# Kernel tuning notes

Hardware: AMD Instinct MI355X
Metric: run time of the kernel (lower is better)

The kernel has to match this reference:

```python
import jax, jax.numpy as jnp
import numpy as np

N_BATCH = 2; N_RAYS = 4096; S_COARSE = 32; S_FINE = 32
FEATURE_DIM = 32; BOX_WARP = 6.0; EPS = 1e-5

_PLANE_AXES = np.array([[[1, 0, 0], [0, 1, 0], [0, 0, 1]],
                        [[1, 0, 0], [0, 0, 1], [0, 1, 0]],
                        [[0, 0, 1], [0, 1, 0], [1, 0, 0]]], dtype=np.float32)
_INV_PLANES = np.linalg.inv(_PLANE_AXES)  # [3,3,3]


def _grid_sample(feat, coords):
    # feat [B,C,H,W], coords [B,M,2] in [-1,1] (x->W, y->H); bilinear, align_corners=False, zero padding
    B, C, H, W = feat.shape
    x = (coords[..., 0] + 1.0) * (W * 0.5) - 0.5
    y = (coords[..., 1] + 1.0) * (H * 0.5) - 0.5
    x0 = jnp.floor(x); y0 = jnp.floor(y)
    wx = x - x0; wy = y - y0
    x0i = x0.astype(jnp.int32); y0i = y0.astype(jnp.int32)

    def corner(fb, yi, xi):
        valid = ((xi >= 0) & (xi < W) & (yi >= 0) & (yi < H)).astype(fb.dtype)
        v = fb[:, jnp.clip(yi, 0, H - 1), jnp.clip(xi, 0, W - 1)]  # [C,M]
        return v * valid[None, :]

    def one(fb, x0b, y0b, wxb, wyb):
        x1b = x0b + 1; y1b = y0b + 1
        return (corner(fb, y0b, x0b) * (1 - wxb) * (1 - wyb)
                + corner(fb, y0b, x1b) * wxb * (1 - wyb)
                + corner(fb, y1b, x0b) * (1 - wxb) * wyb
                + corner(fb, y1b, x1b) * wxb * wyb)  # [C,M]

    return jax.vmap(one)(feat, x0i, y0i, wx, wy)  # [B,C,M]


def _sample_from_planes(planes, coords):
    # planes [N,3,C,H,W], coords [N,M,3] -> [N,3,M,C]
    N, n_planes, C, H, W = planes.shape
    M = coords.shape[1]
    c = coords * (2.0 / BOX_WARP)
    proj = jnp.einsum('nmc,pcd->npmd', c, jnp.asarray(_INV_PLANES))[..., :2]  # [N,3,M,2]
    out = _grid_sample(planes.reshape(N * n_planes, C, H, W), proj.reshape(N * n_planes, M, 2))
    return out.reshape(N, n_planes, C, M).transpose(0, 1, 3, 2)


def _decoder(feat, W1, b1, W2, b2):
    # OSGDecoder: Linear -> softplus -> Linear; rgb sigmoid-squashed, sigma raw
    h = jax.nn.softplus(feat @ W1 + b1)
    o = h @ W2 + b2
    rgb = jax.nn.sigmoid(o[..., 1:]) * (1 + 2 * 0.001) - 0.001
    sigma = o[..., 0:1]
    return rgb, sigma


def _run_model(planes, coords, W1, b1, W2, b2, beta):
    sf = _sample_from_planes(planes, coords).mean(axis=1)  # [N,M,C]
    rgb, raw_sigma = _decoder(sf, W1, b1, W2, b2)
    pred_sdf = raw_sigma
    # template SDF stand-in (external FLAME tex_feature net): sphere SDF
    tsdf = jnp.linalg.norm(coords, axis=-1, keepdims=True) - 0.5
    sigma = raw_sigma + tsdf
    density = jax.nn.sigmoid(-sigma / beta) / beta  # sdf_activation(-sigma)
    return rgb, density, pred_sdf


def _ray_march(colors, densities, depths):
    deltas = depths[:, :, 1:] - depths[:, :, :-1]
    c_mid = 0.5 * (colors[:, :, :-1] + colors[:, :, 1:])
    d_mid = 0.5 * (densities[:, :, :-1] + densities[:, :, 1:])
    z_mid = 0.5 * (depths[:, :, :-1] + depths[:, :, 1:])
    alpha = 1.0 - jnp.exp(-d_mid * deltas)
    shifted = jnp.concatenate([jnp.ones_like(alpha[:, :, :1]), 1.0 - alpha + 1e-10], axis=2)
    weights = alpha * jnp.cumprod(shifted, axis=2)[:, :, :-1]
    comp_rgb = jnp.sum(weights * c_mid, axis=2) * 2.0 - 1.0
    w_tot = jnp.sum(weights, axis=2)
    comp_depth = jnp.sum(weights * z_mid, axis=2) / w_tot
    comp_depth = jnp.nan_to_num(comp_depth, nan=jnp.inf)
    comp_depth = jnp.clip(comp_depth, depths.min(), depths.max())
    return comp_rgb, comp_depth, weights


def _sample_pdf(bins, weights, u):
    n_w = weights.shape[-1]
    w = weights + EPS
    pdf = w / jnp.sum(w, axis=-1, keepdims=True)
    cdf = jnp.cumsum(pdf, axis=-1)
    cdf = jnp.concatenate([jnp.zeros_like(cdf[:, :1]), cdf], axis=-1)
    inds = jax.vmap(lambda c, uu: jnp.searchsorted(c, uu, side='right'))(cdf, u)
    below = jnp.maximum(inds - 1, 0)
    above = jnp.minimum(inds, n_w)
    cdf0 = jnp.take_along_axis(cdf, below, axis=-1)
    cdf1 = jnp.take_along_axis(cdf, above, axis=-1)
    b0 = jnp.take_along_axis(bins, below, axis=-1)
    b1v = jnp.take_along_axis(bins, above, axis=-1)
    denom = cdf1 - cdf0
    denom = jnp.where(denom < EPS, 1.0, denom)
    return b0 + (u - cdf0) / denom * (b1v - b0)


def _sample_importance(z_vals, weights, u):
    B, R, S, _ = z_vals.shape
    z = z_vals.reshape(B * R, S)
    w = weights.reshape(B * R, -1)  # S-1
    # torch max_pool1d(k=2,s=1,pad=1) then avg_pool1d(k=2,s=1)
    neg = jnp.full_like(w[:, :1], -1e10)
    wp = jnp.concatenate([neg, w, neg], axis=-1)
    m = jnp.maximum(wp[:, :-1], wp[:, 1:])  # len S
    w_sm = 0.5 * (m[:, :-1] + m[:, 1:]) + 0.01  # len S-1
    z_mid = 0.5 * (z[:, :-1] + z[:, 1:])  # len S-1
    s = _sample_pdf(z_mid, w_sm[:, 1:-1], u)
    return jax.lax.stop_gradient(s.reshape(B, R, -1, 1))


def reference(planes, ray_origins, ray_directions, hit_min_depth, hit_max_depth, jitter, u_importance, W1, b1, W2, b2, sigmoid_beta, hit_mask):
    N, M, _ = ray_origins.shape
    beta = jnp.maximum(sigmoid_beta, 0.002)
    mask = hit_mask.astype(planes.dtype)[:, :, None, None]  # [N,M,1,1]
    hmin = jnp.where(mask == 0, hit_min_depth.min(), hit_min_depth)
    hmax = jnp.where(mask == 0, hit_max_depth.max(), hit_max_depth)
    base = jnp.linspace(0.0, 1.0, S_COARSE, dtype=planes.dtype).reshape(1, 1, S_COARSE, 1)
    span = hmax - hmin
    d_coarse = (base + jitter * span / S_COARSE) * span + hmin  # [N,M,S,1]

    def eval_points(depths):
        coords = ray_origins[:, :, None, :] + depths * ray_directions[:, :, None, :]
        S = depths.shape[2]
        rgb, dens, psdf = _run_model(planes, coords.reshape(N, M * S, 3), W1, b1, W2, b2, beta)
        # masked scatter-back into dense buffers == multiply by hit mask
        rgb = rgb.reshape(N, M, S, FEATURE_DIM) * mask
        dens = dens.reshape(N, M, S, 1) * mask
        return rgb, dens, psdf

    rgb_c, dens_c, psdf_c = eval_points(d_coarse)
    _, _, w_c = _ray_march(rgb_c, dens_c, d_coarse)
    d_fine = _sample_importance(d_coarse, w_c, u_importance)
    rgb_f, dens_f, psdf_f = eval_points(d_fine)

    all_d = jnp.concatenate([d_coarse, d_fine], axis=2)
    all_c = jnp.concatenate([rgb_c, rgb_f], axis=2)
    all_s = jnp.concatenate([dens_c, dens_f], axis=2)
    idx = jnp.argsort(all_d, axis=2)
    all_d = jnp.take_along_axis(all_d, idx, axis=2)
    all_c = jnp.take_along_axis(all_c, jnp.broadcast_to(idx, all_c.shape), axis=2)
    all_s = jnp.take_along_axis(all_s, jnp.broadcast_to(idx, all_s.shape), axis=2)

    rgb_final, depth_final, weights = _ray_march(all_c, all_s, all_d)
    all_pred_sdf = jnp.concatenate([psdf_c, psdf_f], axis=1)
    return rgb_final, depth_final, weights, all_pred_sdf


def setup_inputs():
    key = jax.random.key(0)
    ks = jax.random.split(key, 12)
    planes = jax.random.normal(ks[0], (N_BATCH, 3, 32, 256, 256), jnp.float32)
    ray_origins = 0.1 * jax.random.normal(ks[1], (N_BATCH, N_RAYS, 3), jnp.float32)
    rd = jax.random.normal(ks[2], (N_BATCH, N_RAYS, 3), jnp.float32)
    ray_directions = rd / jnp.linalg.norm(rd, axis=-1, keepdims=True)
    hit_min_depth = 0.8 + 0.4 * jax.random.uniform(ks[3], (N_BATCH, N_RAYS, 1, 1), jnp.float32)
    hit_max_depth = hit_min_depth + 0.5 + jax.random.uniform(ks[4], (N_BATCH, N_RAYS, 1, 1), jnp.float32)
    jitter = jax.random.uniform(ks[5], (N_BATCH, N_RAYS, S_COARSE, 1), jnp.float32)
    u_importance = jax.random.uniform(ks[6], (N_BATCH * N_RAYS, S_FINE), jnp.float32)
    W1 = 0.05 * jax.random.normal(ks[7], (32, 64), jnp.float32)
    b1 = jnp.zeros((64,), jnp.float32)
    W2 = 0.05 * jax.random.normal(ks[8], (64, 1 + FEATURE_DIM), jnp.float32)
    b2 = jnp.zeros((1 + FEATURE_DIM,), jnp.float32)
    sigmoid_beta = 0.1 * jnp.ones((1,), jnp.float32)
    hit_mask = jax.random.randint(ks[9], (N_BATCH, N_RAYS), 0, 2, jnp.int32)
    return {'planes': planes, 'ray_origins': ray_origins, 'ray_directions': ray_directions,
            'hit_min_depth': hit_min_depth, 'hit_max_depth': hit_max_depth, 'jitter': jitter,
            'u_importance': u_importance, 'W1': W1, 'b1': b1, 'W2': W2, 'b2': b2,
            'sigmoid_beta': sigmoid_beta, 'hit_mask': hit_mask}
```

## Files before the change

kernel.cpp:

```cpp
#include <hip/hip_runtime.h>
#include <hip/hip_bf16.h>
#include <math.h>
#include <stddef.h>

typedef unsigned int u32;
typedef unsigned short u16;
typedef unsigned long long u64;

#define NRAYS 8192
#define NSAMP 262144

__device__ __forceinline__ float fa(float a,float b){ return __fadd_rn(a,b); }
__device__ __forceinline__ float fs(float a,float b){ return __fsub_rn(a,b); }
__device__ __forceinline__ float fm(float a,float b){ return __fmul_rn(a,b); }
__device__ __forceinline__ float fdv(float a,float b){ return __fdiv_rn(a,b); }

__device__ __forceinline__ double exp_d(double x){
  const double LOG2E  = 1.4426950408889634074;
  const double LN2_HI = 6.93147180369123816490e-01;
  const double LN2_LO = 1.90821492927058770002e-10;
  double kd = rint(x * LOG2E);
  if (kd >  200.0) return INFINITY;
  if (kd < -200.0) return 0.0;
  int k = (int)kd;
  double r = fma(-kd, LN2_HI, x);
  r = fma(-kd, LN2_LO, r);
  double p = 1.0/39916800.0;
  p = fma(p, r, 1.0/3628800.0);
  p = fma(p, r, 1.0/362880.0);
  p = fma(p, r, 1.0/40320.0);
  p = fma(p, r, 1.0/5040.0);
  p = fma(p, r, 1.0/720.0);
  p = fma(p, r, 1.0/120.0);
  p = fma(p, r, 1.0/24.0);
  p = fma(p, r, 1.0/6.0);
  p = fma(p, r, 0.5);
  p = fma(p, r, 1.0);
  p = fma(p, r, 1.0);
  u64 sb = ((u64)(k + 1023)) << 52;
  return p * __longlong_as_double((long long)sb);
}
__device__ __forceinline__ float exf(float x){ return (float)exp_d((double)x); }
__device__ __forceinline__ float sigm(float x){
  if (x >= 0.f){ float e = exf(-x); return fdv(1.f, fa(1.f, e)); }
  float e = exf(x); return fdv(e, fa(1.f, e));
}
__device__ __forceinline__ float sigm_fast(float x){
  return 1.f/(1.f + __expf(-x));
}
__device__ __forceinline__ u16 f2b(float f){
  u32 x = __float_as_uint(f);
  return (u16)((x + 0x7fffu + ((x>>16)&1u)) >> 16);
}
__device__ __forceinline__ u32 fenc(float f){ u32 b=__float_as_uint(f); return (b&0x80000000u)? ~b : (b|0x80000000u); }
__device__ __forceinline__ float fdec(u32 k){ u32 b=(k&0x80000000u)? (k^0x80000000u) : ~k; return __uint_as_float(b); }

__global__ void k_init(const float* __restrict__ hmin, const float* __restrict__ hmax,
                       const float* __restrict__ W1, float* __restrict__ scal,
                       float* __restrict__ W1t){
  __shared__ float smn[256], smx[256];
  int t = threadIdx.x;
  float mn = 1e30f, mx = -1e30f;
  for (int i=t;i<NRAYS;i+=256){ mn=fminf(mn,hmin[i]); mx=fmaxf(mx,hmax[i]); }
  smn[t]=mn; smx[t]=mx; __syncthreads();
  for(int s=128;s>0;s>>=1){
    if(t<s){ smn[t]=fminf(smn[t],smn[t+s]); smx[t]=fmaxf(smx[t],smx[t+s]); }
    __syncthreads();
  }
  if(t==0){
    scal[0]=smn[0]; scal[1]=smx[0];
    ((u32*)scal)[2]=0xFFFFFFFFu;
    ((u32*)scal)[3]=0u;
  }
  for(int i=t;i<2048;i+=256){ int j=i>>5, c=i&31; W1t[i]=W1[c*64+j]; }
}

__global__ void __launch_bounds__(256) k_tr(const float* __restrict__ pl, float* __restrict__ pt){
  int t = blockIdx.x*256 + threadIdx.x;
  int x  = t & 255;
  int c4 = ((t>>8)&7)<<2;
  int y  = (t>>11)&255;
  int np = t>>19;
  const float* ip = pl + (((size_t)(np*32+c4))<<16) + (y<<8) + x;
  float4 o;
  o.x = ip[0];
  o.y = ip[65536];
  o.z = ip[131072];
  o.w = ip[196608];
  *reinterpret_cast<float4*>(pt + ((((size_t)(np<<8|y))<<8|x)<<5) + c4) = o;
}

template<int PHASE>
__global__ void __launch_bounds__(256) k_eval(
  const float* __restrict__ pt, const float* __restrict__ ro, const float* __restrict__ rd,
  const float* __restrict__ hmin, const float* __restrict__ hmax,
  const float* __restrict__ jitter, const int* __restrict__ hitmask,
  const float* __restrict__ W1t, const float* __restrict__ b1,
  const float* __restrict__ W2, const float* __restrict__ b2,
  const float* __restrict__ sb, float* __restrict__ scal,
  float* __restrict__ dep, float* __restrict__ dens_out, u16* __restrict__ rgb_out,
  float* __restrict__ out_psdf)
{
  int idx = blockIdx.x*256 + threadIdx.x;
  int ray = idx >> 5;
  int s   = idx & 31;
  int n   = ray >> 12;
  int msk = hitmask[ray];

  float d;
  if (PHASE==0){
    float hmn = msk ? hmin[ray] : scal[0];
    float hmx = msk ? hmax[ray] : scal[1];
    float span = fs(hmx, hmn);
    float jit  = jitter[idx];
    float base = (float)((double)s * (1.0/31.0));
    if (s==31) base = 1.0f;
    float t1 = fdv(fm(jit, span), 32.0f);
    d = fa(fm(fa(base, t1), span), hmn);
    dep[idx] = d;
    float dm=d, dM=d;
#pragma unroll
    for (int m=1;m<64;m<<=1){ dm=fminf(dm,__shfl_xor(dm,m)); dM=fmaxf(dM,__shfl_xor(dM,m)); }
    if ((threadIdx.x & 63)==0){
      atomicMin(((u32*)scal)+2, fenc(dm));
      atomicMax(((u32*)scal)+3, fenc(dM));
    }
  } else {
    d = dep[idx];
  }

  float ox=ro[ray*3+0], oy=ro[ray*3+1], oz=ro[ray*3+2];
  float dx=rd[ray*3+0], dy=rd[ray*3+1], dz=rd[ray*3+2];
  float px = fa(ox, fm(d,dx)), py = fa(oy, fm(d,dy)), pz = fa(oz, fm(d,dz));
  float nrm = __fsqrt_rn(fa(fa(fm(px,px),fm(py,py)),fm(pz,pz)));
  float tsdf = fs(nrm, 0.5f);
  const float sc2 = (float)(2.0/6.0);
  float cx=fm(px,sc2), cy=fm(py,sc2), cz=fm(pz,sc2);

  float feat[32];
#pragma unroll
  for(int c=0;c<32;c++) feat[c]=0.f;

#pragma unroll
  for (int p=0;p<3;p++){
    float u = (p==2)?cz:cx;
    float v = (p==1)?cz:cy;
    float fx = fs(fm(fa(u,1.f),128.f),0.5f);
    float fy = fs(fm(fa(v,1.f),128.f),0.5f);
    float x0f = floorf(fx), y0f = floorf(fy);
    float wx = fs(fx,x0f), wy = fs(fy,y0f);
    float ax0 = fs(1.f,wx), ax1 = wx, ay0 = fs(1.f,wy), ay1 = wy;
    int x0, y0;
    {
      x0 = (x0f >= 2.1e9f) ? 2147483647 : ((x0f <= -2.1e9f) ? (-2147483647-1) : (int)x0f);
      y0 = (y0f >= 2.1e9f) ? 2147483647 : ((y0f <= -2.1e9f) ? (-2147483647-1) : (int)y0f);
    }
    int x1=x0+1, y1=y0+1;
    bool vx0 = (x0>=0 && x0<256), vx1 = (x1>=0 && x1<256);
    bool vy0 = (y0>=0 && y0<256), vy1 = (y1>=0 && y1<256);
    bool ok00 = vx0&&vy0, ok01 = vx1&&vy0, ok10 = vx0&&vy1, ok11 = vx1&&vy1;
    int cx0=min(max(x0,0),255), cx1=min(max(x1,0),255);
    int cy0=min(max(y0,0),255), cy1=min(max(y1,0),255);
    int npl = n*3+p;
    size_t pb = ((size_t)npl)<<16;
    const float4* t00 = (const float4*)(pt + ((pb + (cy0<<8) + cx0)<<5));
    const float4* t01 = (const float4*)(pt + ((pb + (cy0<<8) + cx1)<<5));
    const float4* t10 = (const float4*)(pt + ((pb + (cy1<<8) + cx0)<<5));
    const float4* t11 = (const float4*)(pt + ((pb + (cy1<<8) + cx1)<<5));
#pragma unroll
    for(int q=0;q<8;q++){
      float4 v00 = t00[q], v01 = t01[q], v10 = t10[q], v11 = t11[q];
      float e0,e1,e2,e3, t_;
#define CORNER_SUM(FLD, OUTI) \
      e0 = ok00 ? v00.FLD : 0.f; e1 = ok01 ? v01.FLD : 0.f; \
      e2 = ok10 ? v10.FLD : 0.f; e3 = ok11 ? v11.FLD : 0.f; \
      t_ = fa(fa(fa(fm(fm(e0,ax0),ay0), fm(fm(e1,ax1),ay0)), fm(fm(e2,ax0),ay1)), fm(fm(e3,ax1),ay1)); \
      feat[q*4+OUTI] = fa(feat[q*4+OUTI], t_);
      CORNER_SUM(x,0) CORNER_SUM(y,1) CORNER_SUM(z,2) CORNER_SUM(w,3)
#undef CORNER_SUM
    }
  }
#pragma unroll
  for(int c=0;c<32;c++) feat[c] = fdv(feat[c], 3.0f);

  float o[33];
#pragma unroll
  for(int k=0;k<33;k++) o[k]=0.f;
#pragma unroll 2
  for(int j=0;j<64;j++){
    float a = 0.f;
#pragma unroll
    for(int c=0;c<32;c++) a = fmaf(feat[c], W1t[j*32+c], a);
    a = fa(a, b1[j]);
    float h = fa(fmaxf(a,0.f), __logf(fa(1.f, __expf(-fabsf(a)))));
#pragma unroll
    for(int k=0;k<33;k++) o[k] = fmaf(h, W2[j*33+k], o[k]);
  }
#pragma unroll
  for(int k=0;k<33;k++) o[k] = fa(o[k], b2[k]);

  float beta = fmaxf(sb[0], 0.002f);
  float raw = o[0];
  out_psdf[((size_t)n<<18) + ((size_t)PHASE<<17) + (size_t)(ray&4095)*32 + s] = raw;
  float sg = fa(raw, tsdf);
  float dens = msk ? fdv(sigm(fdv(-sg, beta)), beta) : 0.f;
  dens_out[idx]=dens;

  u16 rv[32];
#pragma unroll
  for(int c=0;c<32;c++){
    float r = msk ? fs(fm(sigm_fast(o[c+1]), 1.002f), 0.001f) : 0.f;
    rv[c]=f2b(r);
  }
  uint4* op = (uint4*)(rgb_out + (size_t)idx*32);
#pragma unroll
  for(int q=0;q<4;q++){
    uint4 w;
    w.x = (u32)rv[q*8+0] | ((u32)rv[q*8+1]<<16);
    w.y = (u32)rv[q*8+2] | ((u32)rv[q*8+3]<<16);
    w.z = (u32)rv[q*8+4] | ((u32)rv[q*8+5]<<16);
    w.w = (u32)rv[q*8+6] | ((u32)rv[q*8+7]<<16);
    op[q]=w;
  }
}

__global__ void __launch_bounds__(64) k_imp(
  const float* __restrict__ dc, const float* __restrict__ dens,
  const float* __restrict__ u_imp, float* __restrict__ df, float* __restrict__ scal)
{
  __shared__ float scdf[64][30];
  __shared__ float szm [64][30];
  int tid = threadIdx.x;
  int ray = blockIdx.x*64 + tid;
  float w[31];
  float dprev = dc[ray*32+0];
  float sprev = dens[ray*32+0];
  float T = 1.f;
#pragma unroll
  for(int i=0;i<31;i++){
    float dn = dc[ray*32+i+1];
    float sn = dens[ray*32+i+1];
    if (i<30) szm[tid][i] = fm(0.5f, fa(dprev,dn));
    float delta = fs(dn,dprev);
    float dm = fm(0.5f, fa(sprev,sn));
    float al = fs(1.f, exf(-fm(dm,delta)));
    w[i] = fm(al,T);
    T = fm(T, fa(fs(1.f,al), 1e-10f));
    dprev=dn; sprev=sn;
  }
  float pdfw[29];
#pragma unroll
  for(int i=0;i<29;i++){
    float m1 = fmaxf(w[i],w[i+1]), m2 = fmaxf(w[i+1],w[i+2]);
    pdfw[i] = fa(fa(fm(0.5f, fa(m1,m2)), 0.01f), 1e-5f);
  }
  float sum;
  {
    float r[8];
#pragma unroll
    for(int j=0;j<8;j++) r[j]=pdfw[j];
#pragma unroll
    for(int j=0;j<8;j++) r[j]=fa(r[j],pdfw[8+j]);
#pragma unroll
    for(int j=0;j<8;j++) r[j]=fa(r[j],pdfw[16+j]);
    sum = fa(fa(fa(r[0],r[1]),fa(r[2],r[3])), fa(fa(r[4],r[5]),fa(r[6],r[7])));
#pragma unroll
    for(int i=24;i<29;i++) sum = fa(sum, pdfw[i]);
  }
  {
    float cacc = 0.f;
    scdf[tid][0] = 0.f;
#pragma unroll
    for(int i=1;i<30;i++){
      cacc = fa(cacc, fdv(pdfw[i-1], sum));
      scdf[tid][i] = cacc;
    }
  }

  float fmn=1e30f, fmx=-1e30f;
  for(int k=0;k<32;k++){
    float u = u_imp[ray*32+k];
    int lo=0, hi=30;
    while(lo<hi){
      int mid=(lo+hi)>>1;
      if (scdf[tid][mid] <= u) lo = mid+1; else hi = mid;
    }
    int ind = lo;
    int below = ind-1;
    int above = (ind>29)?29:ind;
    float cdf0 = scdf[tid][below];
    float cdf1 = scdf[tid][above];
    float b0   = szm [tid][below];
    float b1v  = szm [tid][above];
    float den = fs(cdf1,cdf0);
    if((double)den < 1e-5) den = 1.f;
    float sres = fa(b0, fm(fdv(fs(u,cdf0),den), fs(b1v,b0)));
    df[ray*32+k]=sres;
    fmn=fminf(fmn,sres); fmx=fmaxf(fmx,sres);
  }
#pragma unroll
  for(int m=1;m<64;m<<=1){ fmn=fminf(fmn,__shfl_xor(fmn,m)); fmx=fmaxf(fmx,__shfl_xor(fmx,m)); }
  if(tid==0){
    atomicMin(((u32*)scal)+2, fenc(fmn));
    atomicMax(((u32*)scal)+3, fenc(fmx));
  }
}

__global__ void __launch_bounds__(256) k_final(
  const float* __restrict__ dc, const float* __restrict__ df,
  const float* __restrict__ densc, const float* __restrict__ densf,
  const u16* __restrict__ rgbc, const u16* __restrict__ rgbf,
  const float* __restrict__ scal,
  float* __restrict__ out_rgb, float* __restrict__ out_depth, float* __restrict__ out_w)
{
  __shared__ float ssd[4][64];
  __shared__ float ssn[4][64];
  __shared__ int   sp [4][64];
  __shared__ float swv[4][64];
  __shared__ float swz[4][64];
  int wid = threadIdx.x>>6, lane = threadIdx.x&63;
  int ray = blockIdx.x*4 + wid;

  float myd = (lane<32)? dc[ray*32+lane]    : df[ray*32+lane-32];
  float myn = (lane<32)? densc[ray*32+lane] : densf[ray*32+lane-32];
  ssd[wid][lane]=myd; __syncthreads();
  int rk=0;
#pragma unroll 8
  for(int j=0;j<64;j++){
    float dj = ssd[wid][j];
    rk += (dj<myd || (dj==myd && j<lane)) ? 1:0;
  }
  __syncthreads();
  ssd[wid][rk]=myd; ssn[wid][rk]=myn; sp[wid][rk]=lane;
  __syncthreads();

  float T=1.f, accr=0.f;
  int j0 = sp[wid][0];
  float cprev = 0.f;
  if (lane<32){
    const u16* cb = (j0<32)? (rgbc+((size_t)ray*32+j0)*32) : (rgbf+((size_t)ray*32+(j0-32))*32);
    cprev = __uint_as_float(((u32)cb[lane])<<16);
  }
  float d0 = ssd[wid][0], n0 = ssn[wid][0];
  for(int s2=0;s2<63;s2++){
    float d1 = ssd[wid][s2+1], n1 = ssn[wid][s2+1];
    float delta = fs(d1,d0);
    float dm = fm(0.5f, fa(n0,n1));
    float al = fs(1.f, exf(-fm(dm,delta)));
    float wv = fm(al,T);
    T = fm(T, fa(fs(1.f,al), 1e-10f));
    if (lane==s2){ swv[wid][s2]=wv; swz[wid][s2]=fm(wv, fm(0.5f, fa(d0,d1))); }
    int j1 = sp[wid][s2+1];
    float cnext = 0.f;
    if (lane<32){
      const u16* cb = (j1<32)? (rgbc+((size_t)ray*32+j1)*32) : (rgbf+((size_t)ray*32+(j1-32))*32);
      cnext = __uint_as_float(((u32)cb[lane])<<16);
    }
    accr = fa(accr, fm(wv, fm(0.5f, fa(cprev,cnext))));
    cprev=cnext; d0=d1; n0=n1;
  }
  __syncthreads();
  if(lane<63) out_w[(size_t)ray*63+lane]=swv[wid][lane];
  if(lane<32) out_rgb[(size_t)ray*32+lane]=fs(fm(accr,2.f),1.f);
  if(lane==0){
    float wsum, zsum;
    {
      float r[8], rz[8];
#pragma unroll
      for(int j=0;j<8;j++){ r[j]=swv[wid][j]; rz[j]=swz[wid][j]; }
      for(int i=8;i<56;i+=8)
#pragma unroll
        for(int j=0;j<8;j++){ r[j]=fa(r[j],swv[wid][i+j]); rz[j]=fa(rz[j],swz[wid][i+j]); }
      wsum = fa(fa(fa(r[0],r[1]),fa(r[2],r[3])), fa(fa(r[4],r[5]),fa(r[6],r[7])));
      zsum = fa(fa(fa(rz[0],rz[1]),fa(rz[2],rz[3])), fa(fa(rz[4],rz[5]),fa(rz[6],rz[7])));
      for(int i=56;i<63;i++){ wsum=fa(wsum,swv[wid][i]); zsum=fa(zsum,swz[wid][i]); }
    }
    float depv = fdv(zsum, wsum);
    if (isnan(depv)) depv = INFINITY;
    float lo = fdec(((const u32*)scal)[2]);
    float hi = fdec(((const u32*)scal)[3]);
    depv = fminf(fmaxf(depv,lo),hi);
    out_depth[ray]=depv;
  }
}

extern "C" void kernel_launch(void* const* d_in, const int* in_sizes, int n_in,
                              void* d_out, int out_size, void* d_ws, size_t ws_size,
                              hipStream_t stream) {
  const float* planes = (const float*)d_in[0];
  const float* ro     = (const float*)d_in[1];
  const float* rdp    = (const float*)d_in[2];
  const float* hmin   = (const float*)d_in[3];
  const float* hmax   = (const float*)d_in[4];
  const float* jitter = (const float*)d_in[5];
  const float* uimp   = (const float*)d_in[6];
  const float* W1     = (const float*)d_in[7];
  const float* b1     = (const float*)d_in[8];
  const float* W2     = (const float*)d_in[9];
  const float* b2     = (const float*)d_in[10];
  const float* sb     = (const float*)d_in[11];
  const int*   hmk    = (const int*)d_in[12];
  float* out = (float*)d_out;
  char* ws = (char*)d_ws;

  size_t off=0;
  auto alloc=[&](size_t bytes){ size_t o=off; off=(off+bytes+255)&~(size_t)255; return o; };
  float* scal = (float*)(ws+alloc(64));
  float* W1t  = (float*)(ws+alloc(2048*4));
  float* pt   = (float*)(ws+alloc((size_t)12582912*4));
  float* dco  = (float*)(ws+alloc((size_t)NSAMP*4));
  float* dfi  = (float*)(ws+alloc((size_t)NSAMP*4));
  float* dnc  = (float*)(ws+alloc((size_t)NSAMP*4));
  float* dnf  = (float*)(ws+alloc((size_t)NSAMP*4));
  u16*   rgc  = (u16*)  (ws+alloc((size_t)NSAMP*32*2));
  u16*   rgf  = (u16*)  (ws+alloc((size_t)NSAMP*32*2));
  (void)in_sizes; (void)n_in; (void)out_size; (void)ws_size;

  float* out_rgb  = out;
  float* out_dep  = out + 262144;
  float* out_w    = out + 270336;
  float* out_psdf = out + 786432;

  k_init<<<dim3(1),dim3(256),0,stream>>>(hmin,hmax,W1,scal,W1t);
  k_tr<<<dim3(12288),dim3(256),0,stream>>>(planes, pt);
  k_eval<0><<<dim3(1024),dim3(256),0,stream>>>(pt,ro,rdp,hmin,hmax,jitter,hmk,W1t,b1,W2,b2,sb,scal,dco,dnc,rgc,out_psdf);
  k_imp<<<dim3(128),dim3(64),0,stream>>>(dco,dnc,uimp,dfi,scal);
  k_eval<1><<<dim3(1024),dim3(256),0,stream>>>(pt,ro,rdp,hmin,hmax,jitter,hmk,W1t,b1,W2,b2,sb,scal,dfi,dnf,rgf,out_psdf);
  k_final<<<dim3(2048),dim3(256),0,stream>>>(dco,dfi,dnc,dnf,rgc,rgf,scal,out_rgb,out_dep,out_w);
}
```

Before: 457.5 us.

## Split each sample's MLP across two threads with shuffle reduction

After: 1.016 ms. +122.0%, slower.

```diff
diff --git a/kernel.cpp b/kernel.cpp
--- a/kernel.cpp
+++ b/kernel.cpp
@@ -101,9 +101,11 @@
   float* __restrict__ dep, float* __restrict__ dens_out, u16* __restrict__ rgb_out,
   float* __restrict__ out_psdf)
 {
-  int idx = blockIdx.x*256 + threadIdx.x;
-  int ray = idx >> 5;
-  int s   = idx & 31;
+  int tid = blockIdx.x*256 + threadIdx.x;
+  int pid = tid >> 1;
+  int hf  = tid & 1;
+  int ray = pid >> 5;
+  int s   = pid & 31;
   int n   = ray >> 12;
   int msk = hitmask[ray];
 
@@ -112,12 +114,12 @@
     float hmn = msk ? hmin[ray] : scal[0];
     float hmx = msk ? hmax[ray] : scal[1];
     float span = fs(hmx, hmn);
-    float jit  = jitter[idx];
+    float jit  = jitter[pid];
     float base = (float)((double)s * (1.0/31.0));
     if (s==31) base = 1.0f;
     float t1 = fdv(fm(jit, span), 32.0f);
     d = fa(fm(fa(base, t1), span), hmn);
-    dep[idx] = d;
+    if (hf==0) dep[pid] = d;
     float dm=d, dM=d;
 #pragma unroll
     for (int m=1;m<64;m<<=1){ dm=fminf(dm,__shfl_xor(dm,m)); dM=fmaxf(dM,__shfl_xor(dM,m)); }
@@ -126,7 +128,7 @@
       atomicMax(((u32*)scal)+3, fenc(dM));
     }
   } else {
-    d = dep[idx];
+    d = dep[pid];
   }
 
   float ox=ro[ray*3+0], oy=ro[ray*3+1], oz=ro[ray*3+2];
@@ -183,38 +185,50 @@
 #pragma unroll
   for(int c=0;c<32;c++) feat[c] = fdv(feat[c], 3.0f);
 
+  float opart[33];
+#pragma unroll
+  for(int k=0;k<33;k++) opart[k]=0.f;
+  {
+    const float* w1b = W1t + (hf<<10);
+    const float* b1b = b1 + (hf<<5);
+    const float* w2b = W2 + (hf<<5)*33;
+#pragma unroll 2
+    for(int jj=0;jj<32;jj++){
+      float a = 0.f;
+      const float* wr = w1b + jj*32;
+#pragma unroll
+      for(int c=0;c<32;c++) a = fmaf(feat[c], wr[c], a);
+      a = fa(a, b1b[jj]);
+      float h = fa(fmaxf(a,0.f), __logf(fa(1.f, __expf(-fabsf(a)))));
+      const float* w2r = w2b + jj*33;
+#pragma unroll
+      for(int k=0;k<33;k++) opart[k] = fmaf(h, w2r[k], opart[k]);
+    }
+  }
   float o[33];
 #pragma unroll
-  for(int k=0;k<33;k++) o[k]=0.f;
-#pragma unroll 2
-  for(int j=0;j<64;j++){
-    float a = 0.f;
-#pragma unroll
-    for(int c=0;c<32;c++) a = fmaf(feat[c], W1t[j*32+c], a);
-    a = fa(a, b1[j]);
-    float h = fa(fmaxf(a,0.f), __logf(fa(1.f, __expf(-fabsf(a)))));
-#pragma unroll
-    for(int k=0;k<33;k++) o[k] = fmaf(h, W2[j*33+k], o[k]);
-  }
-#pragma unroll
-  for(int k=0;k<33;k++) o[k] = fa(o[k], b2[k]);
+  for(int k=0;k<33;k++){
+    float t_ = fa(opart[k], __shfl_xor(opart[k],1));
+    o[k] = fa(t_, b2[k]);
+  }
 
   float beta = fmaxf(sb[0], 0.002f);
   float raw = o[0];
-  out_psdf[((size_t)n<<18) + ((size_t)PHASE<<17) + (size_t)(ray&4095)*32 + s] = raw;
   float sg = fa(raw, tsdf);
-  float dens = msk ? fdv(sigm(fdv(-sg, beta)), beta) : 0.f;
-  dens_out[idx]=dens;
-
-  u16 rv[32];
-#pragma unroll
-  for(int c=0;c<32;c++){
-    float r = msk ? fs(fm(sigm_fast(o[c+1]), 1.002f), 0.001f) : 0.f;
+  if (hf==0){
+    out_psdf[((size_t)n<<18) + ((size_t)PHASE<<17) + (size_t)(ray&4095)*32 + s] = raw;
+    dens_out[pid] = msk ? fdv(sigm(fdv(-sg, beta)), beta) : 0.f;
+  }
+
+  u16 rv[16];
+#pragma unroll
+  for(int c=0;c<16;c++){
+    float r = msk ? fs(fm(sigm_fast(o[hf*16+c+1]), 1.002f), 0.001f) : 0.f;
     rv[c]=f2b(r);
   }
-  uint4* op = (uint4*)(rgb_out + (size_t)idx*32);
-#pragma unroll
-  for(int q=0;q<4;q++){
+  uint4* op = (uint4*)(rgb_out + (size_t)pid*32 + hf*16);
+#pragma unroll
+  for(int q=0;q<2;q++){
     uint4 w;
     w.x = (u32)rv[q*8+0] | ((u32)rv[q*8+1]<<16);
     w.y = (u32)rv[q*8+2] | ((u32)rv[q*8+3]<<16);
@@ -423,8 +437,8 @@
 
   k_init<<<dim3(1),dim3(256),0,stream>>>(hmin,hmax,W1,scal,W1t);
   k_tr<<<dim3(12288),dim3(256),0,stream>>>(planes, pt);
-  k_eval<0><<<dim3(1024),dim3(256),0,stream>>>(pt,ro,rdp,hmin,hmax,jitter,hmk,W1t,b1,W2,b2,sb,scal,dco,dnc,rgc,out_psdf);
+  k_eval<0><<<dim3(2048),dim3(256),0,stream>>>(pt,ro,rdp,hmin,hmax,jitter,hmk,W1t,b1,W2,b2,sb,scal,dco,dnc,rgc,out_psdf);
   k_imp<<<dim3(128),dim3(64),0,stream>>>(dco,dnc,uimp,dfi,scal);
-  k_eval<1><<<dim3(1024),dim3(256),0,stream>>>(pt,ro,rdp,hmin,hmax,jitter,hmk,W1t,b1,W2,b2,sb,scal,dfi,dnf,rgf,out_psdf);
+  k_eval<1><<<dim3(2048),dim3(256),0,stream>>>(pt,ro,rdp,hmin,hmax,jitter,hmk,W1t,b1,W2,b2,sb,scal,dfi,dnf,rgf,out_psdf);
   k_final<<<dim3(2048),dim3(256),0,stream>>>(dco,dfi,dnc,dnf,rgc,rgf,scal,out_rgb,out_dep,out_w);
 }
```

## Split fused eval into half-channel sampling kernel and separate MLP decode kernel

Applied to the files above, without the earlier changes.

After: 681.8 us. 1.49x slower.

```diff
diff --git a/kernel.cpp b/kernel.cpp
--- a/kernel.cpp
+++ b/kernel.cpp
@@ -91,19 +91,17 @@
 }
 
 template<int PHASE>
-__global__ void __launch_bounds__(256) k_eval(
+__global__ void __launch_bounds__(256) k_sample(
   const float* __restrict__ pt, const float* __restrict__ ro, const float* __restrict__ rd,
   const float* __restrict__ hmin, const float* __restrict__ hmax,
   const float* __restrict__ jitter, const int* __restrict__ hitmask,
-  const float* __restrict__ W1t, const float* __restrict__ b1,
-  const float* __restrict__ W2, const float* __restrict__ b2,
-  const float* __restrict__ sb, float* __restrict__ scal,
-  float* __restrict__ dep, float* __restrict__ dens_out, u16* __restrict__ rgb_out,
-  float* __restrict__ out_psdf)
+  float* __restrict__ scal, float* __restrict__ dep, float* __restrict__ feat_ws)
 {
-  int idx = blockIdx.x*256 + threadIdx.x;
-  int ray = idx >> 5;
-  int s   = idx & 31;
+  int tid = blockIdx.x*256 + threadIdx.x;
+  int pid = tid >> 1;
+  int hf  = tid & 1;
+  int ray = pid >> 5;
+  int s   = pid & 31;
   int n   = ray >> 12;
   int msk = hitmask[ray];
 
@@ -112,12 +110,12 @@
     float hmn = msk ? hmin[ray] : scal[0];
     float hmx = msk ? hmax[ray] : scal[1];
     float span = fs(hmx, hmn);
-    float jit  = jitter[idx];
+    float jit  = jitter[pid];
     float base = (float)((double)s * (1.0/31.0));
     if (s==31) base = 1.0f;
     float t1 = fdv(fm(jit, span), 32.0f);
     d = fa(fm(fa(base, t1), span), hmn);
-    dep[idx] = d;
+    if (hf==0) dep[pid] = d;
     float dm=d, dM=d;
 #pragma unroll
     for (int m=1;m<64;m<<=1){ dm=fminf(dm,__shfl_xor(dm,m)); dM=fmaxf(dM,__shfl_xor(dM,m)); }
@@ -126,20 +124,18 @@
       atomicMax(((u32*)scal)+3, fenc(dM));
     }
   } else {
-    d = dep[idx];
+    d = dep[pid];
   }
 
   float ox=ro[ray*3+0], oy=ro[ray*3+1], oz=ro[ray*3+2];
   float dx=rd[ray*3+0], dy=rd[ray*3+1], dz=rd[ray*3+2];
   float px = fa(ox, fm(d,dx)), py = fa(oy, fm(d,dy)), pz = fa(oz, fm(d,dz));
-  float nrm = __fsqrt_rn(fa(fa(fm(px,px),fm(py,py)),fm(pz,pz)));
-  float tsdf = fs(nrm, 0.5f);
   const float sc2 = (float)(2.0/6.0);
   float cx=fm(px,sc2), cy=fm(py,sc2), cz=fm(pz,sc2);
 
-  float feat[32];
-#pragma unroll
-  for(int c=0;c<32;c++) feat[c]=0.f;
+  float feat[16];
+#pragma unroll
+  for(int c=0;c<16;c++) feat[c]=0.f;
 
 #pragma unroll
   for (int p=0;p<3;p++){
@@ -163,12 +159,13 @@
     int cy0=min(max(y0,0),255), cy1=min(max(y1,0),255);
     int npl = n*3+p;
     size_t pb = ((size_t)npl)<<16;
-    const float4* t00 = (const float4*)(pt + ((pb + (cy0<<8) + cx0)<<5));
-    const float4* t01 = (const float4*)(pt + ((pb + (cy0<<8) + cx1)<<5));
-    const float4* t10 = (const float4*)(pt + ((pb + (cy1<<8) + cx0)<<5));
-    const float4* t11 = (const float4*)(pt + ((pb + (cy1<<8) + cx1)<<5));
-#pragma unroll
-    for(int q=0;q<8;q++){
+    int qof = hf<<4;
+    const float4* t00 = (const float4*)(pt + ((pb + (cy0<<8) + cx0)<<5) + qof);
+    const float4* t01 = (const float4*)(pt + ((pb + (cy0<<8) + cx1)<<5) + qof);
+    const float4* t10 = (const float4*)(pt + ((pb + (cy1<<8) + cx0)<<5) + qof);
+    const float4* t11 = (const float4*)(pt + ((pb + (cy1<<8) + cx1)<<5) + qof);
+#pragma unroll
+    for(int q=0;q<4;q++){
       float4 v00 = t00[q], v01 = t01[q], v10 = t10[q], v11 = t11[q];
       float e0,e1,e2,e3, t_;
 #define CORNER_SUM(FLD, OUTI) \
@@ -180,8 +177,50 @@
 #undef CORNER_SUM
     }
   }
-#pragma unroll
-  for(int c=0;c<32;c++) feat[c] = fdv(feat[c], 3.0f);
+  float4* fw = (float4*)(feat_ws + ((size_t)pid<<5) + (hf<<4));
+#pragma unroll
+  for(int q=0;q<4;q++){
+    float4 o4;
+    o4.x = fdv(feat[q*4+0], 3.0f);
+    o4.y = fdv(feat[q*4+1], 3.0f);
+    o4.z = fdv(feat[q*4+2], 3.0f);
+    o4.w = fdv(feat[q*4+3], 3.0f);
+    fw[q] = o4;
+  }
+}
+
+template<int PHASE>
+__global__ void __launch_bounds__(256) k_decode(
+  const float* __restrict__ feat_ws, const float* __restrict__ ro, const float* __restrict__ rd,
+  const int* __restrict__ hitmask,
+  const float* __restrict__ W1t, const float* __restrict__ b1,
+  const float* __restrict__ W2, const float* __restrict__ b2,
+  const float* __restrict__ sb,
+  const float* __restrict__ dep, float* __restrict__ dens_out, u16* __restrict__ rgb_out,
+  float* __restrict__ out_psdf)
+{
+  int idx = blockIdx.x*256 + threadIdx.x;
+  int ray = idx >> 5;
+  int s   = idx & 31;
+  int n   = ray >> 12;
+  int msk = hitmask[ray];
+  float d = dep[idx];
+
+  float ox=ro[ray*3+0], oy=ro[ray*3+1], oz=ro[ray*3+2];
+  float dx=rd[ray*3+0], dy=rd[ray*3+1], dz=rd[ray*3+2];
+  float px = fa(ox, fm(d,dx)), py = fa(oy, fm(d,dy)), pz = fa(oz, fm(d,dz));
+  float nrm = __fsqrt_rn(fa(fa(fm(px,px),fm(py,py)),fm(pz,pz)));
+  float tsdf = fs(nrm, 0.5f);
+
+  float feat[32];
+  {
+    const float4* fr = (const float4*)(feat_ws + ((size_t)idx<<5));
+#pragma unroll
+    for(int q=0;q<8;q++){
+      float4 v = fr[q];
+      feat[q*4+0]=v.x; feat[q*4+1]=v.y; feat[q*4+2]=v.z; feat[q*4+3]=v.w;
+    }
+  }
 
   float o[33];
 #pragma unroll
@@ -408,6 +447,7 @@
   float* scal = (float*)(ws+alloc(64));
   float* W1t  = (float*)(ws+alloc(2048*4));
   float* pt   = (float*)(ws+alloc((size_t)12582912*4));
+  float* featw= (float*)(ws+alloc((size_t)NSAMP*32*4));
   float* dco  = (float*)(ws+alloc((size_t)NSAMP*4));
   float* dfi  = (float*)(ws+alloc((size_t)NSAMP*4));
   float* dnc  = (float*)(ws+alloc((size_t)NSAMP*4));
@@ -423,8 +463,10 @@
 
   k_init<<<dim3(1),dim3(256),0,stream>>>(hmin,hmax,W1,scal,W1t);
   k_tr<<<dim3(12288),dim3(256),0,stream>>>(planes, pt);
-  k_eval<0><<<dim3(1024),dim3(256),0,stream>>>(pt,ro,rdp,hmin,hmax,jitter,hmk,W1t,b1,W2,b2,sb,scal,dco,dnc,rgc,out_psdf);
+  k_sample<0><<<dim3(2048),dim3(256),0,stream>>>(pt,ro,rdp,hmin,hmax,jitter,hmk,scal,dco,featw);
+  k_decode<0><<<dim3(1024),dim3(256),0,stream>>>(featw,ro,rdp,hmk,W1t,b1,W2,b2,sb,dco,dnc,rgc,out_psdf);
   k_imp<<<dim3(128),dim3(64),0,stream>>>(dco,dnc,uimp,dfi,scal);
-  k_eval<1><<<dim3(1024),dim3(256),0,stream>>>(pt,ro,rdp,hmin,hmax,jitter,hmk,W1t,b1,W2,b2,sb,scal,dfi,dnf,rgf,out_psdf);
+  k_sample<1><<<dim3(2048),dim3(256),0,stream>>>(pt,ro,rdp,hmin,hmax,jitter,hmk,scal,dfi,featw);
+  k_decode<1><<<dim3(1024),dim3(256),0,stream>>>(featw,ro,rdp,hmk,W1t,b1,W2,b2,sb,dfi,dnf,rgf,out_psdf);
   k_final<<<dim3(2048),dim3(256),0,stream>>>(dco,dfi,dnc,dnf,rgc,rgf,scal,out_rgb,out_dep,out_w);
 }
```

## Sort rays by Morton-coded direction and swizzle eval blocks for locality

Applied to the files above, without the earlier changes.

Result: slower. 569.4 us (+24.5%).

```diff
diff --git a/kernel.cpp b/kernel.cpp
--- a/kernel.cpp
+++ b/kernel.cpp
@@ -75,6 +75,43 @@
   for(int i=t;i<2048;i+=256){ int j=i>>5, c=i&31; W1t[i]=W1[c*64+j]; }
 }
 
+__device__ __forceinline__ u32 part3(u32 v){
+  v &= 0x3FFu;
+  v = (v | (v<<16)) & 0x30000FFu;
+  v = (v | (v<<8))  & 0x300F00Fu;
+  v = (v | (v<<4))  & 0x30C30C3u;
+  v = (v | (v<<2))  & 0x9249249u;
+  return v;
+}
+__global__ void __launch_bounds__(1024) k_sort(const float* __restrict__ rd, u32* __restrict__ perm){
+  __shared__ u64 buf[NRAYS];
+  int t = threadIdx.x;
+  for (int i=t;i<NRAYS;i+=1024){
+    float x = rd[i*3+0], y = rd[i*3+1], z = rd[i*3+2];
+    u32 kx = (u32)fminf(fmaxf((x+1.f)*511.5f,0.f),1023.f);
+    u32 ky = (u32)fminf(fmaxf((y+1.f)*511.5f,0.f),1023.f);
+    u32 kz = (u32)fminf(fmaxf((z+1.f)*511.5f,0.f),1023.f);
+    u32 m = (part3(kx)<<2) | (part3(ky)<<1) | part3(kz);
+    u32 key = ((u32)(i>>12)<<30) | m;
+    buf[i] = ((u64)key<<32) | (u32)i;
+  }
+  __syncthreads();
+  for (int k=2;k<=NRAYS;k<<=1){
+    for (int j=k>>1;j>0;j>>=1){
+      for (int i=t;i<NRAYS;i+=1024){
+        int ixj = i ^ j;
+        if (ixj > i){
+          u64 a = buf[i], b = buf[ixj];
+          bool up = ((i & k) == 0);
+          if ((up && a > b) || (!up && a < b)){ buf[i]=b; buf[ixj]=a; }
+        }
+      }
+      __syncthreads();
+    }
+  }
+  for (int i=t;i<NRAYS;i+=1024) perm[i] = (u32)(buf[i] & 0xFFFFFFFFu);
+}
+
 __global__ void __launch_bounds__(256) k_tr(const float* __restrict__ pl, float* __restrict__ pt){
   int t = blockIdx.x*256 + threadIdx.x;
   int x  = t & 255;
@@ -95,29 +132,34 @@
   const float* __restrict__ pt, const float* __restrict__ ro, const float* __restrict__ rd,
   const float* __restrict__ hmin, const float* __restrict__ hmax,
   const float* __restrict__ jitter, const int* __restrict__ hitmask,
+  const u32* __restrict__ perm,
   const float* __restrict__ W1t, const float* __restrict__ b1,
   const float* __restrict__ W2, const float* __restrict__ b2,
   const float* __restrict__ sb, float* __restrict__ scal,
   float* __restrict__ dep, float* __restrict__ dens_out, u16* __restrict__ rgb_out,
   float* __restrict__ out_psdf)
 {
-  int idx = blockIdx.x*256 + threadIdx.x;
-  int ray = idx >> 5;
-  int s   = idx & 31;
-  int n   = ray >> 12;
-  int msk = hitmask[ray];
+  int bid = blockIdx.x;
+  int swz = (bid & 7)*128 + (bid >> 3);
+  int pidl = swz*256 + threadIdx.x;
+  int rayp = pidl >> 5;
+  int s    = pidl & 31;
+  int ray  = (int)perm[rayp];
+  int pid  = (ray<<5) | s;
+  int n    = ray >> 12;
+  int msk  = hitmask[ray];
 
   float d;
   if (PHASE==0){
     float hmn = msk ? hmin[ray] : scal[0];
     float hmx = msk ? hmax[ray] : scal[1];
     float span = fs(hmx, hmn);
-    float jit  = jitter[idx];
+    float jit  = jitter[pid];
     float base = (float)((double)s * (1.0/31.0));
     if (s==31) base = 1.0f;
     float t1 = fdv(fm(jit, span), 32.0f);
     d = fa(fm(fa(base, t1), span), hmn);
-    dep[idx] = d;
+    dep[pid] = d;
     float dm=d, dM=d;
 #pragma unroll
     for (int m=1;m<64;m<<=1){ dm=fminf(dm,__shfl_xor(dm,m)); dM=fmaxf(dM,__shfl_xor(dM,m)); }
@@ -126,7 +168,7 @@
       atomicMax(((u32*)scal)+3, fenc(dM));
     }
   } else {
-    d = dep[idx];
+    d = dep[pid];
   }
 
   float ox=ro[ray*3+0], oy=ro[ray*3+1], oz=ro[ray*3+2];
@@ -204,7 +246,7 @@
   out_psdf[((size_t)n<<18) + ((size_t)PHASE<<17) + (size_t)(ray&4095)*32 + s] = raw;
   float sg = fa(raw, tsdf);
   float dens = msk ? fdv(sigm(fdv(-sg, beta)), beta) : 0.f;
-  dens_out[idx]=dens;
+  dens_out[pid]=dens;
 
   u16 rv[32];
 #pragma unroll
@@ -212,7 +254,7 @@
     float r = msk ? fs(fm(sigm_fast(o[c+1]), 1.002f), 0.001f) : 0.f;
     rv[c]=f2b(r);
   }
-  uint4* op = (uint4*)(rgb_out + (size_t)idx*32);
+  uint4* op = (uint4*)(rgb_out + (size_t)pid*32);
 #pragma unroll
   for(int q=0;q<4;q++){
     uint4 w;
@@ -317,7 +359,7 @@
   __shared__ float ssn[4][64];
   __shared__ int   sp [4][64];
   __shared__ float swv[4][64];
-  __shared__ float swz[4][64];
+  __shared__ float swz2[4][64];
   int wid = threadIdx.x>>6, lane = threadIdx.x&63;
   int ray = blockIdx.x*4 + wid;
 
@@ -349,7 +391,7 @@
     float al = fs(1.f, exf(-fm(dm,delta)));
     float wv = fm(al,T);
     T = fm(T, fa(fs(1.f,al), 1e-10f));
-    if (lane==s2){ swv[wid][s2]=wv; swz[wid][s2]=fm(wv, fm(0.5f, fa(d0,d1))); }
+    if (lane==s2){ swv[wid][s2]=wv; swz2[wid][s2]=fm(wv, fm(0.5f, fa(d0,d1))); }
     int j1 = sp[wid][s2+1];
     float cnext = 0.f;
     if (lane<32){
@@ -367,13 +409,13 @@
     {
       float r[8], rz[8];
 #pragma unroll
-      for(int j=0;j<8;j++){ r[j]=swv[wid][j]; rz[j]=swz[wid][j]; }
+      for(int j=0;j<8;j++){ r[j]=swv[wid][j]; rz[j]=swz2[wid][j]; }
       for(int i=8;i<56;i+=8)
 #pragma unroll
-        for(int j=0;j<8;j++){ r[j]=fa(r[j],swv[wid][i+j]); rz[j]=fa(rz[j],swz[wid][i+j]); }
+        for(int j=0;j<8;j++){ r[j]=fa(r[j],swv[wid][i+j]); rz[j]=fa(rz[j],swz2[wid][i+j]); }
       wsum = fa(fa(fa(r[0],r[1]),fa(r[2],r[3])), fa(fa(r[4],r[5]),fa(r[6],r[7])));
       zsum = fa(fa(fa(rz[0],rz[1]),fa(rz[2],rz[3])), fa(fa(rz[4],rz[5]),fa(rz[6],rz[7])));
-      for(int i=56;i<63;i++){ wsum=fa(wsum,swv[wid][i]); zsum=fa(zsum,swz[wid][i]); }
+      for(int i=56;i<63;i++){ wsum=fa(wsum,swv[wid][i]); zsum=fa(zsum,swz2[wid][i]); }
     }
     float depv = fdv(zsum, wsum);
     if (isnan(depv)) depv = INFINITY;
@@ -407,6 +449,7 @@
   auto alloc=[&](size_t bytes){ size_t o=off; off=(off+bytes+255)&~(size_t)255; return o; };
   float* scal = (float*)(ws+alloc(64));
   float* W1t  = (float*)(ws+alloc(2048*4));
+  u32*   perm = (u32*)  (ws+alloc(NRAYS*4));
   float* pt   = (float*)(ws+alloc((size_t)12582912*4));
   float* dco  = (float*)(ws+alloc((size_t)NSAMP*4));
   float* dfi  = (float*)(ws+alloc((size_t)NSAMP*4));
@@ -422,9 +465,10 @@
   float* out_psdf = out + 786432;
 
   k_init<<<dim3(1),dim3(256),0,stream>>>(hmin,hmax,W1,scal,W1t);
+  k_sort<<<dim3(1),dim3(1024),0,stream>>>(rdp, perm);
   k_tr<<<dim3(12288),dim3(256),0,stream>>>(planes, pt);
-  k_eval<0><<<dim3(1024),dim3(256),0,stream>>>(pt,ro,rdp,hmin,hmax,jitter,hmk,W1t,b1,W2,b2,sb,scal,dco,dnc,rgc,out_psdf);
+  k_eval<0><<<dim3(1024),dim3(256),0,stream>>>(pt,ro,rdp,hmin,hmax,jitter,hmk,perm,W1t,b1,W2,b2,sb,scal,dco,dnc,rgc,out_psdf);
   k_imp<<<dim3(128),dim3(64),0,stream>>>(dco,dnc,uimp,dfi,scal);
-  k_eval<1><<<dim3(1024),dim3(256),0,stream>>>(pt,ro,rdp,hmin,hmax,jitter,hmk,W1t,b1,W2,b2,sb,scal,dfi,dnf,rgf,out_psdf);
+  k_eval<1><<<dim3(1024),dim3(256),0,stream>>>(pt,ro,rdp,hmin,hmax,jitter,hmk,perm,W1t,b1,W2,b2,sb,scal,dfi,dnf,rgf,out_psdf);
   k_final<<<dim3(2048),dim3(256),0,stream>>>(dco,dfi,dnc,dnf,rgc,rgf,scal,out_rgb,out_dep,out_w);
 }
```
